# Kernel optimization log

Hardware: AMD Instinct MI355X
Metric: run time of the kernel (lower is better)

## Reference

```python
import jax, jax.numpy as jnp
import numpy as np

SC, ST, B, D, H, E, F, TOPK = 2048, 2048, 4, 256, 4, 8, 1024, 2
AUXW = 0.01
EPS = 1e-5


def setup_inputs() -> dict:
    key = jax.random.key(0)
    ks = jax.random.split(key, 16)
    s = 0.02
    n = lambda k, shp: (jax.random.normal(k, shp, jnp.float32) * s)
    z = lambda shp: jnp.zeros(shp, jnp.float32)
    o = lambda shp: jnp.ones(shp, jnp.float32)
    return {
        "x_context": jax.random.normal(ks[0], (SC, B, D), jnp.float32),
        "x_target": jax.random.normal(ks[1], (ST, B, D), jnp.float32),
        # shared self/cross attention (separate_att=False)
        "Wq": n(ks[2], (D, D)), "Wk": n(ks[3], (D, D)), "Wv": n(ks[4], (D, D)),
        "bq": z(D), "bk": z(D), "bv": z(D),
        "Wo": n(ks[5], (D, D)), "bo": z(D),
        # MoE gating + stacked 2-layer expert MLPs (D -> F -> D)
        "Wg": n(ks[6], (D, E)), "bg": z(E),
        "W1": n(ks[7], (E, D, F)), "b1": z((E, F)),
        "W2": n(ks[8], (E, F, D)), "b2": z((E, D)),
        # four post-LayerNorms
        "g_c1": o(D), "b_c1": z(D), "g_c2": o(D), "b_c2": z(D),
        "g_t1": o(D), "b_t1": z(D), "g_t2": o(D), "b_t2": z(D),
    }


def _ln(x, g, b):
    mu = x.mean(-1, keepdims=True)
    var = ((x - mu) ** 2).mean(-1, keepdims=True)
    return (x - mu) * jax.lax.rsqrt(var + EPS) * g + b


def _mha(q_in, kv, Wq, Wk, Wv, bq, bk, bv, Wo, bo):
    Sq, Bt, Dm = q_in.shape
    Sk = kv.shape[0]
    dh = Dm // H
    q = (q_in @ Wq + bq).reshape(Sq, Bt, H, dh)
    k = (kv @ Wk + bk).reshape(Sk, Bt, H, dh)
    v = (kv @ Wv + bv).reshape(Sk, Bt, H, dh)
    scores = jnp.einsum('qbhd,kbhd->bhqk', q, k) / jnp.asarray(np.sqrt(dh), q.dtype)
    attn = jax.nn.softmax(scores, axis=-1)
    out = jnp.einsum('bhqk,kbhd->qbhd', attn, v).reshape(Sq, Bt, Dm)
    return out @ Wo + bo


def _moe(x, Wg, bg, W1, b1, W2, b2):
    shp = x.shape
    xf = x.reshape(-1, shp[-1])          # [T, D]
    T = xf.shape[0]
    probs = jax.nn.softmax(xf @ Wg + bg, axis=-1)   # [T, E]
    gv, gi = jax.lax.top_k(probs, TOPK)
    gv = gv / gv.sum(-1, keepdims=True)
    # dense combine weights: gate value if expert selected else 0
    comb = jnp.zeros((T, E), xf.dtype).at[jnp.arange(T)[:, None], gi].add(gv)
    out = jnp.zeros_like(xf)
    for e in range(E):                    # fixed small expert loop
        h = jax.nn.relu(xf @ W1[e] + b1[e])
        out = out + (h @ W2[e] + b2[e]) * comb[:, e:e + 1]
    counts = probs.sum(0)
    frac = counts / counts.sum()
    aux = E * jnp.sum(frac * probs.mean(0))
    return out.reshape(shp), aux


def reference(x_context, x_target, Wq, Wk, Wv, bq, bk, bv, Wo, bo,
              Wg, bg, W1, b1, W2, b2,
              g_c1, b_c1, g_c2, b_c2, g_t1, b_t1, g_t2, b_t2):
    # context self-attention (post-norm)
    a = _mha(x_context, x_context, Wq, Wk, Wv, bq, bk, bv, Wo, bo)
    xc = _ln(a + x_context, g_c1, b_c1)
    f, aux1 = _moe(xc, Wg, bg, W1, b1, W2, b2)
    xc = _ln(f + xc, g_c2, b_c2)
    # target cross-attention over context (shared attention weights)
    a = _mha(x_target, xc, Wq, Wk, Wv, bq, bk, bv, Wo, bo)
    xt = _ln(a + x_target, g_t1, b_t1)
    f, aux2 = _moe(xt, Wg, bg, W1, b1, W2, b2)
    xt = _ln(f + xt, g_t2, b_t2)
    aux = AUXW * (aux1 + aux2)
    return xc, xt, aux
```

## Files before the change

kernel.cpp:

```cpp
#include <hip/hip_runtime.h>
#include <hip/hip_bf16.h>

typedef _Float16 f16_t;
typedef _Float16 f16x8 __attribute__((ext_vector_type(8)));
typedef float f32x4 __attribute__((ext_vector_type(4)));

template<bool BIAS, bool OUTF16>
__global__ __launch_bounds__(256) void gemm16_kernel(
    const f16_t* __restrict__ A, const f16_t* __restrict__ B, void* __restrict__ Cv,
    const float* __restrict__ bias, int M, int N, int K, int lda, int ldb, int ldc)
{
    __shared__ f16_t As[64][72];
    __shared__ f16_t Bs[64][72];
    const int m0 = blockIdx.y * 64, n0 = blockIdx.x * 64;
    const int t = threadIdx.x, wave = t >> 6, lane = t & 63;
    const int wr = (wave >> 1) * 32, wc = (wave & 1) * 32;
    const int lr = lane & 15, kg = lane >> 4;
    const int sr = t >> 2, sc = (t & 3) * 16;
    const f16_t* arp = A + (long long)(m0 + sr) * lda;
    const f16_t* brp = B + (long long)(n0 + sr) * ldb;

    f32x4 acc[2][2] = {};
    for (int k0 = 0; k0 < K; k0 += 64) {
        *reinterpret_cast<f16x8*>(&As[sr][sc])     = *reinterpret_cast<const f16x8*>(&arp[k0 + sc]);
        *reinterpret_cast<f16x8*>(&As[sr][sc + 8]) = *reinterpret_cast<const f16x8*>(&arp[k0 + sc + 8]);
        *reinterpret_cast<f16x8*>(&Bs[sr][sc])     = *reinterpret_cast<const f16x8*>(&brp[k0 + sc]);
        *reinterpret_cast<f16x8*>(&Bs[sr][sc + 8]) = *reinterpret_cast<const f16x8*>(&brp[k0 + sc + 8]);
        __syncthreads();
        #pragma unroll
        for (int c = 0; c < 2; c++) {
            f16x8 a0 = *reinterpret_cast<const f16x8*>(&As[wr + lr][c * 32 + kg * 8]);
            f16x8 a1 = *reinterpret_cast<const f16x8*>(&As[wr + 16 + lr][c * 32 + kg * 8]);
            f16x8 b0 = *reinterpret_cast<const f16x8*>(&Bs[wc + lr][c * 32 + kg * 8]);
            f16x8 b1 = *reinterpret_cast<const f16x8*>(&Bs[wc + 16 + lr][c * 32 + kg * 8]);
            acc[0][0] = __builtin_amdgcn_mfma_f32_16x16x32_f16(a0, b0, acc[0][0], 0, 0, 0);
            acc[0][1] = __builtin_amdgcn_mfma_f32_16x16x32_f16(a0, b1, acc[0][1], 0, 0, 0);
            acc[1][0] = __builtin_amdgcn_mfma_f32_16x16x32_f16(a1, b0, acc[1][0], 0, 0, 0);
            acc[1][1] = __builtin_amdgcn_mfma_f32_16x16x32_f16(a1, b1, acc[1][1], 0, 0, 0);
        }
        __syncthreads();
    }
    #pragma unroll
    for (int mi = 0; mi < 2; mi++)
        #pragma unroll
        for (int ni = 0; ni < 2; ni++)
            #pragma unroll
            for (int r = 0; r < 4; r++) {
                const int row = m0 + wr + mi * 16 + kg * 4 + r;
                const int col = n0 + wc + ni * 16 + lr;
                float v = acc[mi][ni][r];
                if constexpr (BIAS) v += bias[col];
                if constexpr (OUTF16) ((f16_t*)Cv)[(long long)row * ldc + col] = (f16_t)v;
                else                  ((float*)Cv)[(long long)row * ldc + col] = v;
            }
}

__global__ __launch_bounds__(256) void qkv_kernel(
    const f16_t* __restrict__ Aq, const f16_t* __restrict__ Akv,
    const f16_t* __restrict__ B0, const f16_t* __restrict__ B1, const f16_t* __restrict__ B2,
    const float* __restrict__ bi0, const float* __restrict__ bi1, const float* __restrict__ bi2,
    f16_t* __restrict__ C0, f16_t* __restrict__ C1, f16_t* __restrict__ C2)
{
    const int zz = blockIdx.z;
    const f16_t* A = (zz == 0) ? Aq : Akv;
    const f16_t* B = (zz == 0) ? B0 : (zz == 1 ? B1 : B2);
    const float* bias = (zz == 0) ? bi0 : (zz == 1 ? bi1 : bi2);
    f16_t* C = (zz == 0) ? C0 : (zz == 1 ? C1 : C2);

    __shared__ f16_t As[64][72];
    __shared__ f16_t Bs[64][72];
    const int m0 = blockIdx.y * 64, n0 = blockIdx.x * 64;
    const int t = threadIdx.x, wave = t >> 6, lane = t & 63;
    const int wr = (wave >> 1) * 32, wc = (wave & 1) * 32;
    const int lr = lane & 15, kg = lane >> 4;
    const int sr = t >> 2, sc = (t & 3) * 16;
    const f16_t* arp = A + (long long)(m0 + sr) * 256;
    const f16_t* brp = B + (long long)(n0 + sr) * 256;

    f32x4 acc[2][2] = {};
    for (int k0 = 0; k0 < 256; k0 += 64) {
        *reinterpret_cast<f16x8*>(&As[sr][sc])     = *reinterpret_cast<const f16x8*>(&arp[k0 + sc]);
        *reinterpret_cast<f16x8*>(&As[sr][sc + 8]) = *reinterpret_cast<const f16x8*>(&arp[k0 + sc + 8]);
        *reinterpret_cast<f16x8*>(&Bs[sr][sc])     = *reinterpret_cast<const f16x8*>(&brp[k0 + sc]);
        *reinterpret_cast<f16x8*>(&Bs[sr][sc + 8]) = *reinterpret_cast<const f16x8*>(&brp[k0 + sc + 8]);
        __syncthreads();
        #pragma unroll
        for (int c = 0; c < 2; c++) {
            f16x8 a0 = *reinterpret_cast<const f16x8*>(&As[wr + lr][c * 32 + kg * 8]);
            f16x8 a1 = *reinterpret_cast<const f16x8*>(&As[wr + 16 + lr][c * 32 + kg * 8]);
            f16x8 b0 = *reinterpret_cast<const f16x8*>(&Bs[wc + lr][c * 32 + kg * 8]);
            f16x8 b1 = *reinterpret_cast<const f16x8*>(&Bs[wc + 16 + lr][c * 32 + kg * 8]);
            acc[0][0] = __builtin_amdgcn_mfma_f32_16x16x32_f16(a0, b0, acc[0][0], 0, 0, 0);
            acc[0][1] = __builtin_amdgcn_mfma_f32_16x16x32_f16(a0, b1, acc[0][1], 0, 0, 0);
            acc[1][0] = __builtin_amdgcn_mfma_f32_16x16x32_f16(a1, b0, acc[1][0], 0, 0, 0);
            acc[1][1] = __builtin_amdgcn_mfma_f32_16x16x32_f16(a1, b1, acc[1][1], 0, 0, 0);
        }
        __syncthreads();
    }
    #pragma unroll
    for (int mi = 0; mi < 2; mi++)
        #pragma unroll
        for (int ni = 0; ni < 2; ni++)
            #pragma unroll
            for (int r = 0; r < 4; r++) {
                const int row = m0 + wr + mi * 16 + kg * 4 + r;
                const int col = n0 + wc + ni * 16 + lr;
                C[(long long)row * 256 + col] = (f16_t)(acc[mi][ni][r] + bias[col]);
            }
}

template<bool GATHER, bool RELU, bool OUTF16>
__global__ __launch_bounds__(256) void moe_gemm16_kernel(
    const f16_t* __restrict__ A, const int* __restrict__ tok_of_slot,
    const f16_t* __restrict__ W, const float* __restrict__ bias,
    void* __restrict__ Cv, const int* __restrict__ ebase,
    int N, int K, int lda, int ldb, int ldc, int wstride, int bstride)
{
    const int m0 = blockIdx.y * 64;
    if (m0 >= ebase[8]) return;
    int e = 0;
    #pragma unroll
    for (int i = 1; i < 8; i++) if (m0 >= ebase[i]) e = i;
    const f16_t* __restrict__ B = W + (long long)e * wstride;
    const float* __restrict__ bs = bias + e * bstride;

    __shared__ f16_t As[64][72];
    __shared__ f16_t Bs[64][72];
    const int n0 = blockIdx.x * 64;
    const int t = threadIdx.x, wave = t >> 6, lane = t & 63;
    const int wr = (wave >> 1) * 32, wc = (wave & 1) * 32;
    const int lr = lane & 15, kg = lane >> 4;
    const int sr = t >> 2, sc = (t & 3) * 16;
    const f16_t* arp;
    if constexpr (GATHER) arp = A + (long long)tok_of_slot[m0 + sr] * lda;
    else                  arp = A + (long long)(m0 + sr) * lda;
    const f16_t* brp = B + (long long)(n0 + sr) * ldb;

    f32x4 acc[2][2] = {};
    for (int k0 = 0; k0 < K; k0 += 64) {
        *reinterpret_cast<f16x8*>(&As[sr][sc])     = *reinterpret_cast<const f16x8*>(&arp[k0 + sc]);
        *reinterpret_cast<f16x8*>(&As[sr][sc + 8]) = *reinterpret_cast<const f16x8*>(&arp[k0 + sc + 8]);
        *reinterpret_cast<f16x8*>(&Bs[sr][sc])     = *reinterpret_cast<const f16x8*>(&brp[k0 + sc]);
        *reinterpret_cast<f16x8*>(&Bs[sr][sc + 8]) = *reinterpret_cast<const f16x8*>(&brp[k0 + sc + 8]);
        __syncthreads();
        #pragma unroll
        for (int c = 0; c < 2; c++) {
            f16x8 a0 = *reinterpret_cast<const f16x8*>(&As[wr + lr][c * 32 + kg * 8]);
            f16x8 a1 = *reinterpret_cast<const f16x8*>(&As[wr + 16 + lr][c * 32 + kg * 8]);
            f16x8 b0 = *reinterpret_cast<const f16x8*>(&Bs[wc + lr][c * 32 + kg * 8]);
            f16x8 b1 = *reinterpret_cast<const f16x8*>(&Bs[wc + 16 + lr][c * 32 + kg * 8]);
            acc[0][0] = __builtin_amdgcn_mfma_f32_16x16x32_f16(a0, b0, acc[0][0], 0, 0, 0);
            acc[0][1] = __builtin_amdgcn_mfma_f32_16x16x32_f16(a0, b1, acc[0][1], 0, 0, 0);
            acc[1][0] = __builtin_amdgcn_mfma_f32_16x16x32_f16(a1, b0, acc[1][0], 0, 0, 0);
            acc[1][1] = __builtin_amdgcn_mfma_f32_16x16x32_f16(a1, b1, acc[1][1], 0, 0, 0);
        }
        __syncthreads();
    }
    #pragma unroll
    for (int mi = 0; mi < 2; mi++)
        #pragma unroll
        for (int ni = 0; ni < 2; ni++)
            #pragma unroll
            for (int r = 0; r < 4; r++) {
                const int row = m0 + wr + mi * 16 + kg * 4 + r;
                const int col = n0 + wc + ni * 16 + lr;
                float v = acc[mi][ni][r] + bs[col];
                if constexpr (RELU) v = fmaxf(v, 0.f);
                if constexpr (OUTF16) ((f16_t*)Cv)[(long long)row * ldc + col] = (f16_t)v;
                else                  ((float*)Cv)[(long long)row * ldc + col] = v;
            }
}

__global__ __launch_bounds__(256) void vtrans_kernel(
    const f16_t* __restrict__ V16, f16_t* __restrict__ VT)
{
    __shared__ f16_t tile[32][33];
    const int z = blockIdx.z;
    const int s0 = blockIdx.x * 32, d0 = blockIdx.y * 32;
    const int tx = threadIdx.x & 31, ty = threadIdx.x >> 5;
    #pragma unroll
    for (int i = 0; i < 32; i += 8)
        tile[ty + i][tx] = V16[(long long)(s0 + ty + i) * 1024 + 64 * z + d0 + tx];
    __syncthreads();
    #pragma unroll
    for (int i = 0; i < 32; i += 8)
        VT[(long long)z * 131072 + (long long)(d0 + ty + i) * 2048 + s0 + tx] = tile[tx][ty + i];
}

__global__ __launch_bounds__(256) void flash_kernel(
    const f16_t* __restrict__ Q16, const f16_t* __restrict__ K16,
    const f16_t* __restrict__ VT, float* __restrict__ Opart,
    float* __restrict__ mlm, float* __restrict__ mll)
{
    __shared__ f16_t Ks[64][72];
    __shared__ f16_t VTs[64][72];
    __shared__ f16_t Ps[4][16][72];

    const int z = blockIdx.y;
    const int c = blockIdx.z;
    const int m0 = blockIdx.x * 64;
    const int t = threadIdx.x, w = t >> 6, lane = t & 63;
    const int lr = lane & 15, kg = lane >> 4;
    const long long cbase = 64LL * z;

    f16x8 qf0, qf1;
    {
        const long long qrow = (long long)(m0 + w * 16 + lr) * 1024 + cbase;
        qf0 = *reinterpret_cast<const f16x8*>(&Q16[qrow + kg * 8]);
        qf1 = *reinterpret_cast<const f16x8*>(&Q16[qrow + 32 + kg * 8]);
        #pragma unroll
        for (int i = 0; i < 8; i++) { qf0[i] *= (f16_t)0.125f; qf1[i] *= (f16_t)0.125f; }
    }

    f32x4 oacc[4] = {};
    float mrun[4] = { -1e30f, -1e30f, -1e30f, -1e30f };
    float lrun[4] = {};

    const int sr = t >> 2, sc = (t & 3) * 16;
    const int nbeg = c * 512;
    for (int n0 = nbeg; n0 < nbeg + 512; n0 += 64) {
        const long long krow = (long long)(n0 + sr) * 1024 + cbase;
        const long long vrow = (long long)z * 131072 + (long long)sr * 2048 + n0;
        *reinterpret_cast<f16x8*>(&Ks[sr][sc])      = *reinterpret_cast<const f16x8*>(&K16[krow + sc]);
        *reinterpret_cast<f16x8*>(&Ks[sr][sc + 8])  = *reinterpret_cast<const f16x8*>(&K16[krow + sc + 8]);
        *reinterpret_cast<f16x8*>(&VTs[sr][sc])     = *reinterpret_cast<const f16x8*>(&VT[vrow + sc]);
        *reinterpret_cast<f16x8*>(&VTs[sr][sc + 8]) = *reinterpret_cast<const f16x8*>(&VT[vrow + sc + 8]);
        __syncthreads();

        float sv[4][4];
        #pragma unroll
        for (int nt = 0; nt < 4; nt++) {
            f32x4 acc = {};
            f16x8 b0 = *reinterpret_cast<const f16x8*>(&Ks[nt * 16 + lr][kg * 8]);
            f16x8 b1 = *reinterpret_cast<const f16x8*>(&Ks[nt * 16 + lr][32 + kg * 8]);
            acc = __builtin_amdgcn_mfma_f32_16x16x32_f16(qf0, b0, acc, 0, 0, 0);
            acc = __builtin_amdgcn_mfma_f32_16x16x32_f16(qf1, b1, acc, 0, 0, 0);
            #pragma unroll
            for (int r = 0; r < 4; r++) sv[nt][r] = acc[r];
        }

        float mnew[4], alpha[4];
        #pragma unroll
        for (int r = 0; r < 4; r++) {
            float rm = fmaxf(fmaxf(sv[0][r], sv[1][r]), fmaxf(sv[2][r], sv[3][r]));
            rm = fmaxf(rm, __shfl_xor(rm, 1));
            rm = fmaxf(rm, __shfl_xor(rm, 2));
            rm = fmaxf(rm, __shfl_xor(rm, 4));
            rm = fmaxf(rm, __shfl_xor(rm, 8));
            mnew[r] = fmaxf(mrun[r], rm);
            alpha[r] = __expf(mrun[r] - mnew[r]);
            mrun[r] = mnew[r];
        }
        #pragma unroll
        for (int nt = 0; nt < 4; nt++)
            #pragma unroll
            for (int r = 0; r < 4; r++) sv[nt][r] = __expf(sv[nt][r] - mnew[r]);
        #pragma unroll
        for (int r = 0; r < 4; r++) {
            float rs = sv[0][r] + sv[1][r] + sv[2][r] + sv[3][r];
            rs += __shfl_xor(rs, 1);
            rs += __shfl_xor(rs, 2);
            rs += __shfl_xor(rs, 4);
            rs += __shfl_xor(rs, 8);
            lrun[r] = lrun[r] * alpha[r] + rs;
        }
        #pragma unroll
        for (int dt = 0; dt < 4; dt++)
            #pragma unroll
            for (int r = 0; r < 4; r++) oacc[dt][r] *= alpha[r];

        #pragma unroll
        for (int nt = 0; nt < 4; nt++)
            #pragma unroll
            for (int r = 0; r < 4; r++)
                Ps[w][kg * 4 + r][nt * 16 + lr] = (f16_t)sv[nt][r];

        f16x8 pa0 = *reinterpret_cast<const f16x8*>(&Ps[w][lr][kg * 8]);
        f16x8 pa1 = *reinterpret_cast<const f16x8*>(&Ps[w][lr][32 + kg * 8]);
        #pragma unroll
        for (int dt = 0; dt < 4; dt++) {
            f16x8 vb0 = *reinterpret_cast<const f16x8*>(&VTs[dt * 16 + lr][kg * 8]);
            f16x8 vb1 = *reinterpret_cast<const f16x8*>(&VTs[dt * 16 + lr][32 + kg * 8]);
            oacc[dt] = __builtin_amdgcn_mfma_f32_16x16x32_f16(pa0, vb0, oacc[dt], 0, 0, 0);
            oacc[dt] = __builtin_amdgcn_mfma_f32_16x16x32_f16(pa1, vb1, oacc[dt], 0, 0, 0);
        }
        __syncthreads();
    }

    float* op = Opart + (long long)c * 2097152;
    const long long orow0 = (long long)(m0 + w * 16) * 1024 + cbase;
    #pragma unroll
    for (int r = 0; r < 4; r++)
        #pragma unroll
        for (int dt = 0; dt < 4; dt++)
            op[orow0 + (long long)(kg * 4 + r) * 1024 + dt * 16 + lr] = oacc[dt][r];
    if (lr == 0) {
        const int b = z >> 2, h = z & 3;
        #pragma unroll
        for (int r = 0; r < 4; r++) {
            const int tok = (m0 + w * 16 + kg * 4 + r) * 4 + b;
            const long long idx = (long long)(c * 4 + h) * 8192 + tok;
            mlm[idx] = mrun[r];
            mll[idx] = lrun[r];
        }
    }
}

__global__ __launch_bounds__(256) void merge_kernel(
    const float* __restrict__ Opart, const float* __restrict__ mlm,
    const float* __restrict__ mll, f16_t* __restrict__ O16)
{
    const int w = threadIdx.x >> 6, lane = threadIdx.x & 63;
    const int trow = blockIdx.x * 4 + w;
    const int h = lane >> 4;
    float m[4], l[4];
    #pragma unroll
    for (int c = 0; c < 4; c++) {
        m[c] = mlm[(long long)(c * 4 + h) * 8192 + trow];
        l[c] = mll[(long long)(c * 4 + h) * 8192 + trow];
    }
    float M = fmaxf(fmaxf(m[0], m[1]), fmaxf(m[2], m[3]));
    float wv[4], L = 0.f;
    #pragma unroll
    for (int c = 0; c < 4; c++) { wv[c] = __expf(m[c] - M); L += wv[c] * l[c]; }
    const float inv = 1.f / L;
    const long long base = (long long)trow * 256 + lane * 4;
    float4 acc = make_float4(0.f, 0.f, 0.f, 0.f);
    #pragma unroll
    for (int c = 0; c < 4; c++) {
        float4 v = *reinterpret_cast<const float4*>(&Opart[(long long)c * 2097152 + base]);
        acc.x += wv[c] * v.x; acc.y += wv[c] * v.y;
        acc.z += wv[c] * v.z; acc.w += wv[c] * v.w;
    }
    f16_t o[4] = { (f16_t)(acc.x * inv), (f16_t)(acc.y * inv),
                   (f16_t)(acc.z * inv), (f16_t)(acc.w * inv) };
    *reinterpret_cast<ulong1*>(&O16[base]) = *reinterpret_cast<ulong1*>(o);
}

__global__ __launch_bounds__(256) void wtrans_kernel(
    const float* __restrict__ in, f16_t* __restrict__ out, int R, int C)
{
    __shared__ float tile[32][33];
    const long long zoff = (long long)blockIdx.z * R * C;
    const int r0 = blockIdx.y * 32, c0 = blockIdx.x * 32;
    const int tx = threadIdx.x & 31, ty = threadIdx.x >> 5;
    #pragma unroll
    for (int i = 0; i < 32; i += 8)
        tile[ty + i][tx] = in[zoff + (long long)(r0 + ty + i) * C + c0 + tx];
    __syncthreads();
    #pragma unroll
    for (int i = 0; i < 32; i += 8)
        out[zoff + (long long)(c0 + ty + i) * R + r0 + tx] = (f16_t)tile[tx][ty + i];
}

__global__ __launch_bounds__(256) void cvt16_kernel(
    const float* __restrict__ in, f16_t* __restrict__ out)
{
    const long long i = ((long long)blockIdx.x * 256 + threadIdx.x) * 4;
    float4 v = *reinterpret_cast<const float4*>(&in[i]);
    f16_t o[4] = { (f16_t)v.x, (f16_t)v.y, (f16_t)v.z, (f16_t)v.w };
    *reinterpret_cast<ulong1*>(&out[i]) = *reinterpret_cast<ulong1*>(o);
}

__global__ __launch_bounds__(256) void ln_kernel(
    const float* __restrict__ in1, const float* __restrict__ in2,
    const float* __restrict__ gamma, const float* __restrict__ beta,
    float* __restrict__ out, f16_t* __restrict__ out16)
{
    const int wave = threadIdx.x >> 6, lane = threadIdx.x & 63;
    const long long row = (long long)blockIdx.x * 4 + wave;
    const long long base = row * 256 + lane * 4;
    float4 a = *reinterpret_cast<const float4*>(&in1[base]);
    float4 b = *reinterpret_cast<const float4*>(&in2[base]);
    float x[4] = { a.x + b.x, a.y + b.y, a.z + b.z, a.w + b.w };
    float s = x[0] + x[1] + x[2] + x[3];
    float s2 = x[0]*x[0] + x[1]*x[1] + x[2]*x[2] + x[3]*x[3];
    #pragma unroll
    for (int o = 32; o; o >>= 1) { s += __shfl_xor(s, o); s2 += __shfl_xor(s2, o); }
    const float mean = s * (1.f / 256.f);
    const float var = s2 * (1.f / 256.f) - mean * mean;
    const float rstd = rsqrtf(var + 1e-5f);
    float4 g = *reinterpret_cast<const float4*>(&gamma[lane * 4]);
    float4 bb = *reinterpret_cast<const float4*>(&beta[lane * 4]);
    const float* gf = reinterpret_cast<const float*>(&g);
    const float* bf = reinterpret_cast<const float*>(&bb);
    float y[4];
    #pragma unroll
    for (int i = 0; i < 4; i++) y[i] = (x[i] - mean) * rstd * gf[i] + bf[i];
    *reinterpret_cast<float4*>(&out[base]) = make_float4(y[0], y[1], y[2], y[3]);
    if (out16) {
        f16_t o[4] = { (f16_t)y[0], (f16_t)y[1], (f16_t)y[2], (f16_t)y[3] };
        *reinterpret_cast<ulong1*>(&out16[base]) = *reinterpret_cast<ulong1*>(o);
    }
}

__global__ __launch_bounds__(256) void gating_kernel(
    const float* __restrict__ X, const float* __restrict__ Wg, const float* __restrict__ bg,
    int* __restrict__ gcount, float* __restrict__ counts,
    int* __restrict__ pos_of_tok, int* __restrict__ exp_of_tok,
    float* __restrict__ gate_of_tok)
{
    __shared__ float WgL[2048];
    __shared__ float cpart[8];
    __shared__ int lcnt[8];
    __shared__ int lbase[8];
    const int t = threadIdx.x;
    for (int i = t; i < 2048; i += 256) WgL[i] = Wg[i];
    if (t < 8) { cpart[t] = 0.f; lcnt[t] = 0; }
    __syncthreads();

    const int tok = blockIdx.x * 256 + t;
    const float* xr = X + (long long)tok * 256;
    float acc[8] = {};
    for (int k = 0; k < 256; k += 4) {
        float4 xv = *reinterpret_cast<const float4*>(xr + k);
        const float* xf = reinterpret_cast<const float*>(&xv);
        #pragma unroll
        for (int i = 0; i < 4; i++) {
            const float xi = xf[i];
            const float* wrow = &WgL[(k + i) * 8];
            #pragma unroll
            for (int e = 0; e < 8; e++) acc[e] += xi * wrow[e];
        }
    }
    float p[8]; float mx = -1e30f;
    #pragma unroll
    for (int e = 0; e < 8; e++) { p[e] = acc[e] + bg[e]; mx = fmaxf(mx, p[e]); }
    float se = 0.f;
    #pragma unroll
    for (int e = 0; e < 8; e++) { p[e] = __expf(p[e] - mx); se += p[e]; }
    const float inv = 1.f / se;
    #pragma unroll
    for (int e = 0; e < 8; e++) { p[e] *= inv; atomicAdd(&cpart[e], p[e]); }

    int i1 = 0;
    #pragma unroll
    for (int e = 1; e < 8; e++) if (p[e] > p[i1]) i1 = e;
    int i2 = (i1 == 0) ? 1 : 0;
    #pragma unroll
    for (int e = 0; e < 8; e++) if (e != i1 && p[e] > p[i2]) i2 = e;
    const float gs = 1.f / (p[i1] + p[i2]);

    const int p1 = atomicAdd(&lcnt[i1], 1);
    const int p2 = atomicAdd(&lcnt[i2], 1);
    __syncthreads();
    if (t < 8) {
        lbase[t] = atomicAdd(&gcount[t], lcnt[t]);
        atomicAdd(&counts[t], cpart[t]);
    }
    __syncthreads();
    pos_of_tok[2 * tok]     = lbase[i1] + p1;
    pos_of_tok[2 * tok + 1] = lbase[i2] + p2;
    exp_of_tok[2 * tok]     = i1;
    exp_of_tok[2 * tok + 1] = i2;
    gate_of_tok[2 * tok]     = p[i1] * gs;
    gate_of_tok[2 * tok + 1] = p[i2] * gs;
}

__global__ void finalize_kernel(const int* __restrict__ gcount, int* __restrict__ ebase)
{
    if (threadIdx.x == 0) {
        int b = 0;
        for (int e = 0; e < 8; e++) { ebase[e] = b; b += (gcount[e] + 63) & ~63; }
        ebase[8] = b;
    }
}

__global__ __launch_bounds__(256) void scatter_kernel(
    const int* __restrict__ pos_of_tok, const int* __restrict__ exp_of_tok,
    const int* __restrict__ ebase, int* __restrict__ tok_of_slot)
{
    const int i = blockIdx.x * 256 + threadIdx.x;
    const int e = exp_of_tok[i];
    tok_of_slot[ebase[e] + pos_of_tok[i]] = i >> 1;
}

__global__ __launch_bounds__(256) void moe_combine_ln_kernel(
    const float* __restrict__ Ys, const float* __restrict__ X1,
    const int* __restrict__ pos_of_tok, const int* __restrict__ exp_of_tok,
    const float* __restrict__ gate_of_tok, const int* __restrict__ ebase,
    const float* __restrict__ gamma, const float* __restrict__ beta,
    float* __restrict__ out, f16_t* __restrict__ out16)
{
    const int wave = threadIdx.x >> 6, lane = threadIdx.x & 63;
    const long long tok = (long long)blockIdx.x * 4 + wave;
    const int e1 = exp_of_tok[2 * tok], e2 = exp_of_tok[2 * tok + 1];
    const long long s1 = ebase[e1] + pos_of_tok[2 * tok];
    const long long s2 = ebase[e2] + pos_of_tok[2 * tok + 1];
    const float gv1 = gate_of_tok[2 * tok], gv2 = gate_of_tok[2 * tok + 1];
    const long long base = tok * 256 + lane * 4;
    float4 y1 = *reinterpret_cast<const float4*>(&Ys[s1 * 256 + lane * 4]);
    float4 y2 = *reinterpret_cast<const float4*>(&Ys[s2 * 256 + lane * 4]);
    float4 xv = *reinterpret_cast<const float4*>(&X1[base]);
    float x[4] = { gv1 * y1.x + gv2 * y2.x + xv.x,
                   gv1 * y1.y + gv2 * y2.y + xv.y,
                   gv1 * y1.z + gv2 * y2.z + xv.z,
                   gv1 * y1.w + gv2 * y2.w + xv.w };
    float s = x[0] + x[1] + x[2] + x[3];
    float s2v = x[0]*x[0] + x[1]*x[1] + x[2]*x[2] + x[3]*x[3];
    #pragma unroll
    for (int o = 32; o; o >>= 1) { s += __shfl_xor(s, o); s2v += __shfl_xor(s2v, o); }
    const float mean = s * (1.f / 256.f);
    const float var = s2v * (1.f / 256.f) - mean * mean;
    const float rstd = rsqrtf(var + 1e-5f);
    float4 g = *reinterpret_cast<const float4*>(&gamma[lane * 4]);
    float4 bb = *reinterpret_cast<const float4*>(&beta[lane * 4]);
    const float* gf = reinterpret_cast<const float*>(&g);
    const float* bf = reinterpret_cast<const float*>(&bb);
    float y[4];
    #pragma unroll
    for (int i = 0; i < 4; i++) y[i] = (x[i] - mean) * rstd * gf[i] + bf[i];
    *reinterpret_cast<float4*>(&out[base]) = make_float4(y[0], y[1], y[2], y[3]);
    if (out16) {
        f16_t o[4] = { (f16_t)y[0], (f16_t)y[1], (f16_t)y[2], (f16_t)y[3] };
        *reinterpret_cast<ulong1*>(&out16[base]) = *reinterpret_cast<ulong1*>(o);
    }
}

__global__ void aux_kernel(const float* __restrict__ counts, float* __restrict__ out)
{
    if (threadIdx.x == 0) {
        float aux = 0.f;
        for (int pzz = 0; pzz < 2; pzz++) {
            const float* c = counts + pzz * 8;
            float tot = 0.f;
            for (int e = 0; e < 8; e++) tot += c[e];
            float s = 0.f;
            for (int e = 0; e < 8; e++) s += (c[e] / tot) * (c[e] * (1.f / 8192.f));
            aux += 8.f * s;
        }
        out[0] = 0.01f * aux;
    }
}

extern "C" void kernel_launch(void* const* d_in, const int* in_sizes, int n_in,
                              void* d_out, int out_size, void* d_ws, size_t ws_size,
                              hipStream_t stream)
{
    const float* Xc  = (const float*)d_in[0];
    const float* Xt  = (const float*)d_in[1];
    const float* Wq  = (const float*)d_in[2];
    const float* Wk  = (const float*)d_in[3];
    const float* Wv  = (const float*)d_in[4];
    const float* bq  = (const float*)d_in[5];
    const float* bk  = (const float*)d_in[6];
    const float* bv  = (const float*)d_in[7];
    const float* Wo  = (const float*)d_in[8];
    const float* bo  = (const float*)d_in[9];
    const float* Wg  = (const float*)d_in[10];
    const float* bg  = (const float*)d_in[11];
    const float* W1  = (const float*)d_in[12];
    const float* b1  = (const float*)d_in[13];
    const float* W2  = (const float*)d_in[14];
    const float* b2  = (const float*)d_in[15];
    const float* g_c1 = (const float*)d_in[16];
    const float* b_c1 = (const float*)d_in[17];
    const float* g_c2 = (const float*)d_in[18];
    const float* b_c2 = (const float*)d_in[19];
    const float* g_t1 = (const float*)d_in[20];
    const float* b_t1 = (const float*)d_in[21];
    const float* g_t2 = (const float*)d_in[22];
    const float* b_t2 = (const float*)d_in[23];

    const long long NTOK = 2097152;
    const int SLOT_MAX = 16896;
    float* dout = (float*)d_out;
    float* xcout = dout;
    float* xtout = dout + NTOK;

    float* ws = (float*)d_ws;
    float* P1 = ws;
    float* X1 = P1 + NTOK;
    float* Ys = X1 + NTOK;
    float* counts      = Ys + (long long)SLOT_MAX * 256;
    float* gate_of_tok = counts + 16;
    float* mlm = gate_of_tok + 16384;
    float* mll = mlm + 131072;
    int* gcount      = (int*)(mll + 131072);
    int* ebase       = gcount + 16;
    int* pos_of_tok  = ebase + 16;
    int* exp_of_tok  = pos_of_tok + 16384;
    int* tok_of_slot = exp_of_tok + 16384;
    f16_t* h16 = (f16_t*)(tok_of_slot + SLOT_MAX);
    f16_t* Xc16 = h16;
    f16_t* Xt16 = Xc16 + NTOK;
    f16_t* xc16 = Xt16 + NTOK;
    f16_t* Q16  = xc16 + NTOK;
    f16_t* K16  = Q16 + NTOK;
    f16_t* V16  = K16 + NTOK;
    f16_t* O16  = V16 + NTOK;
    f16_t* X116 = O16 + NTOK;
    f16_t* VT   = X116 + NTOK;
    f16_t* Hs16 = VT + NTOK;
    f16_t* WqT  = Hs16 + (long long)SLOT_MAX * 1024;
    f16_t* WkT  = WqT + 65536;
    f16_t* WvT  = WkT + 65536;
    f16_t* WoT  = WvT + 65536;
    f16_t* W1T  = WoT + 65536;
    f16_t* W2T  = W1T + 2097152;
    float* Opart = (float*)Hs16;

    hipMemsetAsync(counts, 0, 16 * sizeof(float), stream);
    hipMemsetAsync(gcount, 0, 16 * sizeof(int), stream);

    cvt16_kernel<<<2048, 256, 0, stream>>>(Xc, Xc16);
    cvt16_kernel<<<2048, 256, 0, stream>>>(Xt, Xt16);
    wtrans_kernel<<<dim3(8, 8, 1), 256, 0, stream>>>(Wq, WqT, 256, 256);
    wtrans_kernel<<<dim3(8, 8, 1), 256, 0, stream>>>(Wk, WkT, 256, 256);
    wtrans_kernel<<<dim3(8, 8, 1), 256, 0, stream>>>(Wv, WvT, 256, 256);
    wtrans_kernel<<<dim3(8, 8, 1), 256, 0, stream>>>(Wo, WoT, 256, 256);
    wtrans_kernel<<<dim3(32, 8, 8), 256, 0, stream>>>(W1, W1T, 256, 1024);
    wtrans_kernel<<<dim3(8, 32, 8), 256, 0, stream>>>(W2, W2T, 1024, 256);

    for (int pass = 0; pass < 2; pass++) {
        const float*  xq    = pass ? Xt   : Xc;
        const f16_t*  xq16  = pass ? Xt16 : Xc16;
        const f16_t*  xkv16 = pass ? xc16 : Xc16;
        const float* g1  = pass ? g_t1 : g_c1;
        const float* be1 = pass ? b_t1 : b_c1;
        const float* g2  = pass ? g_t2 : g_c2;
        const float* be2 = pass ? b_t2 : b_c2;
        float* cnt = counts + pass * 8;
        int* gcnt  = gcount + pass * 8;
        float* oln = pass ? xtout : xcout;
        f16_t* oln16 = pass ? nullptr : xc16;

        qkv_kernel<<<dim3(4, 128, 3), 256, 0, stream>>>(
            xq16, xkv16, WqT, WkT, WvT, bq, bk, bv, Q16, K16, V16);

        vtrans_kernel<<<dim3(64, 2, 16), 256, 0, stream>>>(V16, VT);
        flash_kernel<<<dim3(32, 16, 4), 256, 0, stream>>>(Q16, K16, VT, Opart, mlm, mll);
        merge_kernel<<<2048, 256, 0, stream>>>(Opart, mlm, mll, O16);

        gemm16_kernel<true,false><<<dim3(4, 128), 256, 0, stream>>>(
            O16, WoT, P1, bo, 8192, 256, 256, 256, 256, 256);
        ln_kernel<<<2048, 256, 0, stream>>>(P1, xq, g1, be1, X1, X116);

        hipMemsetAsync(tok_of_slot, 0, SLOT_MAX * sizeof(int), stream);
        gating_kernel<<<32, 256, 0, stream>>>(X1, Wg, bg, gcnt, cnt,
                                              pos_of_tok, exp_of_tok, gate_of_tok);
        finalize_kernel<<<1, 64, 0, stream>>>(gcnt, ebase);
        scatter_kernel<<<64, 256, 0, stream>>>(pos_of_tok, exp_of_tok, ebase, tok_of_slot);
        moe_gemm16_kernel<true,true,true><<<dim3(16, 264), 256, 0, stream>>>(
            X116, tok_of_slot, W1T, b1, Hs16, ebase,
            1024, 256, 256, 256, 1024, 262144, 1024);
        moe_gemm16_kernel<false,false,false><<<dim3(4, 264), 256, 0, stream>>>(
            Hs16, nullptr, W2T, b2, Ys, ebase,
            256, 1024, 1024, 1024, 256, 262144, 256);
        moe_combine_ln_kernel<<<2048, 256, 0, stream>>>(
            Ys, X1, pos_of_tok, exp_of_tok, gate_of_tok, ebase, g2, be2, oln, oln16);
    }

    aux_kernel<<<1, 64, 0, stream>>>(counts, dout + 2 * NTOK);
}
```

Baseline: 591.8 us.

## Merge setup launches, use f16 flash partials, and share K/V shared-memory tile

Several unrelated changes. The two input conversions are fused into one launch, the four attention weight transposes are fused into one launch, and the two small memsets are collapsed into one by making counts and gcount adjacent. The per-pass memset of tok_of_slot is dropped; the gather instead masks the token index to stay in bounds. The flash kernel now stores partial outputs in f16 instead of f32, which halves partial traffic into the merge kernel at some precision cost. It also reuses one shared tile for K and then V, adding an extra barrier per iteration, with a launch-bounds occupancy hint.

```diff
diff --git a/kernel.cpp b/kernel.cpp
--- a/kernel.cpp
+++ b/kernel.cpp
@@ -2,6 +2,7 @@
 #include <hip/hip_bf16.h>
 
 typedef _Float16 f16_t;
+typedef _Float16 f16x4v __attribute__((ext_vector_type(4)));
 typedef _Float16 f16x8 __attribute__((ext_vector_type(8)));
 typedef float f32x4 __attribute__((ext_vector_type(4)));
 
@@ -132,7 +133,7 @@
     const int lr = lane & 15, kg = lane >> 4;
     const int sr = t >> 2, sc = (t & 3) * 16;
     const f16_t* arp;
-    if constexpr (GATHER) arp = A + (long long)tok_of_slot[m0 + sr] * lda;
+    if constexpr (GATHER) arp = A + (long long)(tok_of_slot[m0 + sr] & 8191) * lda;
     else                  arp = A + (long long)(m0 + sr) * lda;
     const f16_t* brp = B + (long long)(n0 + sr) * ldb;
 
@@ -187,13 +188,12 @@
         VT[(long long)z * 131072 + (long long)(d0 + ty + i) * 2048 + s0 + tx] = tile[tx][ty + i];
 }
 
-__global__ __launch_bounds__(256) void flash_kernel(
+__global__ __launch_bounds__(256, 6) void flash_kernel(
     const f16_t* __restrict__ Q16, const f16_t* __restrict__ K16,
-    const f16_t* __restrict__ VT, float* __restrict__ Opart,
+    const f16_t* __restrict__ VT, f16_t* __restrict__ Opart,
     float* __restrict__ mlm, float* __restrict__ mll)
 {
-    __shared__ f16_t Ks[64][72];
-    __shared__ f16_t VTs[64][72];
+    __shared__ f16_t KVs[64][72];
     __shared__ f16_t Ps[4][16][72];
 
     const int z = blockIdx.y;
@@ -220,19 +220,16 @@
     const int nbeg = c * 512;
     for (int n0 = nbeg; n0 < nbeg + 512; n0 += 64) {
         const long long krow = (long long)(n0 + sr) * 1024 + cbase;
-        const long long vrow = (long long)z * 131072 + (long long)sr * 2048 + n0;
-        *reinterpret_cast<f16x8*>(&Ks[sr][sc])      = *reinterpret_cast<const f16x8*>(&K16[krow + sc]);
-        *reinterpret_cast<f16x8*>(&Ks[sr][sc + 8])  = *reinterpret_cast<const f16x8*>(&K16[krow + sc + 8]);
-        *reinterpret_cast<f16x8*>(&VTs[sr][sc])     = *reinterpret_cast<const f16x8*>(&VT[vrow + sc]);
-        *reinterpret_cast<f16x8*>(&VTs[sr][sc + 8]) = *reinterpret_cast<const f16x8*>(&VT[vrow + sc + 8]);
+        *reinterpret_cast<f16x8*>(&KVs[sr][sc])     = *reinterpret_cast<const f16x8*>(&K16[krow + sc]);
+        *reinterpret_cast<f16x8*>(&KVs[sr][sc + 8]) = *reinterpret_cast<const f16x8*>(&K16[krow + sc + 8]);
         __syncthreads();
 
         float sv[4][4];
         #pragma unroll
         for (int nt = 0; nt < 4; nt++) {
             f32x4 acc = {};
-            f16x8 b0 = *reinterpret_cast<const f16x8*>(&Ks[nt * 16 + lr][kg * 8]);
-            f16x8 b1 = *reinterpret_cast<const f16x8*>(&Ks[nt * 16 + lr][32 + kg * 8]);
+            f16x8 b0 = *reinterpret_cast<const f16x8*>(&KVs[nt * 16 + lr][kg * 8]);
+            f16x8 b1 = *reinterpret_cast<const f16x8*>(&KVs[nt * 16 + lr][32 + kg * 8]);
             acc = __builtin_amdgcn_mfma_f32_16x16x32_f16(qf0, b0, acc, 0, 0, 0);
             acc = __builtin_amdgcn_mfma_f32_16x16x32_f16(qf1, b1, acc, 0, 0, 0);
             #pragma unroll
@@ -275,25 +272,32 @@
             for (int r = 0; r < 4; r++)
                 Ps[w][kg * 4 + r][nt * 16 + lr] = (f16_t)sv[nt][r];
 
+        __syncthreads();
+
+        const long long vrow = (long long)z * 131072 + (long long)sr * 2048 + n0;
+        *reinterpret_cast<f16x8*>(&KVs[sr][sc])     = *reinterpret_cast<const f16x8*>(&VT[vrow + sc]);
+        *reinterpret_cast<f16x8*>(&KVs[sr][sc + 8]) = *reinterpret_cast<const f16x8*>(&VT[vrow + sc + 8]);
+        __syncthreads();
+
         f16x8 pa0 = *reinterpret_cast<const f16x8*>(&Ps[w][lr][kg * 8]);
         f16x8 pa1 = *reinterpret_cast<const f16x8*>(&Ps[w][lr][32 + kg * 8]);
         #pragma unroll
         for (int dt = 0; dt < 4; dt++) {
-            f16x8 vb0 = *reinterpret_cast<const f16x8*>(&VTs[dt * 16 + lr][kg * 8]);
-            f16x8 vb1 = *reinterpret_cast<const f16x8*>(&VTs[dt * 16 + lr][32 + kg * 8]);
+            f16x8 vb0 = *reinterpret_cast<const f16x8*>(&KVs[dt * 16 + lr][kg * 8]);
+            f16x8 vb1 = *reinterpret_cast<const f16x8*>(&KVs[dt * 16 + lr][32 + kg * 8]);
             oacc[dt] = __builtin_amdgcn_mfma_f32_16x16x32_f16(pa0, vb0, oacc[dt], 0, 0, 0);
             oacc[dt] = __builtin_amdgcn_mfma_f32_16x16x32_f16(pa1, vb1, oacc[dt], 0, 0, 0);
         }
         __syncthreads();
     }
 
-    float* op = Opart + (long long)c * 2097152;
+    f16_t* op = Opart + (long long)c * 2097152;
     const long long orow0 = (long long)(m0 + w * 16) * 1024 + cbase;
     #pragma unroll
     for (int r = 0; r < 4; r++)
         #pragma unroll
         for (int dt = 0; dt < 4; dt++)
-            op[orow0 + (long long)(kg * 4 + r) * 1024 + dt * 16 + lr] = oacc[dt][r];
+            op[orow0 + (long long)(kg * 4 + r) * 1024 + dt * 16 + lr] = (f16_t)oacc[dt][r];
     if (lr == 0) {
         const int b = z >> 2, h = z & 3;
         #pragma unroll
@@ -307,7 +311,7 @@
 }
 
 __global__ __launch_bounds__(256) void merge_kernel(
-    const float* __restrict__ Opart, const float* __restrict__ mlm,
+    const f16_t* __restrict__ Opart, const float* __restrict__ mlm,
     const float* __restrict__ mll, f16_t* __restrict__ O16)
 {
     const int w = threadIdx.x >> 6, lane = threadIdx.x & 63;
@@ -325,15 +329,15 @@
     for (int c = 0; c < 4; c++) { wv[c] = __expf(m[c] - M); L += wv[c] * l[c]; }
     const float inv = 1.f / L;
     const long long base = (long long)trow * 256 + lane * 4;
-    float4 acc = make_float4(0.f, 0.f, 0.f, 0.f);
+    float acc[4] = {};
     #pragma unroll
     for (int c = 0; c < 4; c++) {
-        float4 v = *reinterpret_cast<const float4*>(&Opart[(long long)c * 2097152 + base]);
-        acc.x += wv[c] * v.x; acc.y += wv[c] * v.y;
-        acc.z += wv[c] * v.z; acc.w += wv[c] * v.w;
-    }
-    f16_t o[4] = { (f16_t)(acc.x * inv), (f16_t)(acc.y * inv),
-                   (f16_t)(acc.z * inv), (f16_t)(acc.w * inv) };
+        f16x4v v = *reinterpret_cast<const f16x4v*>(&Opart[(long long)c * 2097152 + base]);
+        #pragma unroll
+        for (int j = 0; j < 4; j++) acc[j] += wv[c] * (float)v[j];
+    }
+    f16_t o[4] = { (f16_t)(acc[0] * inv), (f16_t)(acc[1] * inv),
+                   (f16_t)(acc[2] * inv), (f16_t)(acc[3] * inv) };
     *reinterpret_cast<ulong1*>(&O16[base]) = *reinterpret_cast<ulong1*>(o);
 }
 
@@ -353,10 +357,34 @@
         out[zoff + (long long)(c0 + ty + i) * R + r0 + tx] = (f16_t)tile[tx][ty + i];
 }
 
+__global__ __launch_bounds__(256) void wtrans4_kernel(
+    const float* __restrict__ W0, const float* __restrict__ W1,
+    const float* __restrict__ W2, const float* __restrict__ W3,
+    f16_t* __restrict__ T0, f16_t* __restrict__ T1,
+    f16_t* __restrict__ T2, f16_t* __restrict__ T3)
+{
+    __shared__ float tile[32][33];
+    const int z = blockIdx.z;
+    const float* in = (z == 0) ? W0 : (z == 1 ? W1 : (z == 2 ? W2 : W3));
+    f16_t* out = (z == 0) ? T0 : (z == 1 ? T1 : (z == 2 ? T2 : T3));
+    const int r0 = blockIdx.y * 32, c0 = blockIdx.x * 32;
+    const int tx = threadIdx.x & 31, ty = threadIdx.x >> 5;
+    #pragma unroll
+    for (int i = 0; i < 32; i += 8)
+        tile[ty + i][tx] = in[(long long)(r0 + ty + i) * 256 + c0 + tx];
+    __syncthreads();
+    #pragma unroll
+    for (int i = 0; i < 32; i += 8)
+        out[(long long)(c0 + ty + i) * 256 + r0 + tx] = (f16_t)tile[tx][ty + i];
+}
+
 __global__ __launch_bounds__(256) void cvt16_kernel(
-    const float* __restrict__ in, f16_t* __restrict__ out)
-{
-    const long long i = ((long long)blockIdx.x * 256 + threadIdx.x) * 4;
+    const float* __restrict__ a, const float* __restrict__ b,
+    f16_t* __restrict__ oa, f16_t* __restrict__ ob)
+{
+    long long i = ((long long)blockIdx.x * 256 + threadIdx.x) * 4;
+    const float* in = a; f16_t* out = oa;
+    if (i >= 2097152) { in = b; out = ob; i -= 2097152; }
     float4 v = *reinterpret_cast<const float4*>(&in[i]);
     f16_t o[4] = { (f16_t)v.x, (f16_t)v.y, (f16_t)v.z, (f16_t)v.w };
     *reinterpret_cast<ulong1*>(&out[i]) = *reinterpret_cast<ulong1*>(o);
@@ -573,11 +601,11 @@
     float* X1 = P1 + NTOK;
     float* Ys = X1 + NTOK;
     float* counts      = Ys + (long long)SLOT_MAX * 256;
-    float* gate_of_tok = counts + 16;
+    int*   gcount      = (int*)(counts + 16);
+    float* gate_of_tok = (float*)(gcount + 16);
     float* mlm = gate_of_tok + 16384;
     float* mll = mlm + 131072;
-    int* gcount      = (int*)(mll + 131072);
-    int* ebase       = gcount + 16;
+    int* ebase       = (int*)(mll + 131072);
     int* pos_of_tok  = ebase + 16;
     int* exp_of_tok  = pos_of_tok + 16384;
     int* tok_of_slot = exp_of_tok + 16384;
@@ -598,17 +626,12 @@
     f16_t* WoT  = WvT + 65536;
     f16_t* W1T  = WoT + 65536;
     f16_t* W2T  = W1T + 2097152;
-    float* Opart = (float*)Hs16;
-
-    hipMemsetAsync(counts, 0, 16 * sizeof(float), stream);
-    hipMemsetAsync(gcount, 0, 16 * sizeof(int), stream);
-
-    cvt16_kernel<<<2048, 256, 0, stream>>>(Xc, Xc16);
-    cvt16_kernel<<<2048, 256, 0, stream>>>(Xt, Xt16);
-    wtrans_kernel<<<dim3(8, 8, 1), 256, 0, stream>>>(Wq, WqT, 256, 256);
-    wtrans_kernel<<<dim3(8, 8, 1), 256, 0, stream>>>(Wk, WkT, 256, 256);
-    wtrans_kernel<<<dim3(8, 8, 1), 256, 0, stream>>>(Wv, WvT, 256, 256);
-    wtrans_kernel<<<dim3(8, 8, 1), 256, 0, stream>>>(Wo, WoT, 256, 256);
+    f16_t* Opart = Hs16;
+
+    hipMemsetAsync(counts, 0, 32 * sizeof(int), stream);
+
+    cvt16_kernel<<<4096, 256, 0, stream>>>(Xc, Xt, Xc16, Xt16);
+    wtrans4_kernel<<<dim3(8, 8, 4), 256, 0, stream>>>(Wq, Wk, Wv, Wo, WqT, WkT, WvT, WoT);
     wtrans_kernel<<<dim3(32, 8, 8), 256, 0, stream>>>(W1, W1T, 256, 1024);
     wtrans_kernel<<<dim3(8, 32, 8), 256, 0, stream>>>(W2, W2T, 1024, 256);
 
@@ -636,7 +659,6 @@
             O16, WoT, P1, bo, 8192, 256, 256, 256, 256, 256);
         ln_kernel<<<2048, 256, 0, stream>>>(P1, xq, g1, be1, X1, X116);
 
-        hipMemsetAsync(tok_of_slot, 0, SLOT_MAX * sizeof(int), stream);
         gating_kernel<<<32, 256, 0, stream>>>(X1, Wg, bg, gcnt, cnt,
                                               pos_of_tok, exp_of_tok, gate_of_tok);
         finalize_kernel<<<1, 64, 0, stream>>>(gcnt, ebase);
```

After: 580.9 us. No clear change (-1.8%).
